# Kernel optimization log

Measured on AMD Instinct MI355X. Metric: run time of the kernel, lower is better.

The kernel has to match this reference:

```python
import jax, jax.numpy as jnp
import numpy as np

NEG_SLOPE = 0.2

def gat_conv(x, src, dst, W, a_src, a_dst, bias, num_nodes, heads, out_ch, concat):
    # x: [N, Fin]; W: [Fin, heads*out_ch]; a_src/a_dst: [heads, out_ch]
    h = (x @ W).reshape(num_nodes, heads, out_ch)            # [N,H,C]
    alpha_s = jnp.einsum('nhc,hc->nh', h, a_src)             # [N,H]
    alpha_d = jnp.einsum('nhc,hc->nh', h, a_dst)             # [N,H]
    e = alpha_s[src] + alpha_d[dst]                          # [E,H]
    e = jnp.where(e > 0, e, NEG_SLOPE * e)                   # LeakyReLU
    # segment softmax over incoming edges per destination node
    m = jax.ops.segment_max(e, dst, num_segments=num_nodes)  # [N,H]
    m = jnp.where(jnp.isfinite(m), m, 0.0)
    ee = jnp.exp(e - m[dst])                                 # [E,H]
    s = jax.ops.segment_sum(ee, dst, num_segments=num_nodes) # [N,H]
    alpha = ee / (s[dst] + 1e-16)                            # [E,H]
    out = jax.ops.segment_sum(h[src] * alpha[:, :, None], dst,
                              num_segments=num_nodes)        # [N,H,C]
    if concat:
        out = out.reshape(num_nodes, heads * out_ch)
    else:
        out = out.mean(axis=1)
    return out + bias


def setup_inputs() -> dict:
    key = jax.random.key(0)
    ks = jax.random.split(key, 10)
    N, E = 50000, 800000
    EMB, HID, HEADS, REPR = 128, 128, 8, 64
    C1 = HID // HEADS  # 16
    x = jax.random.normal(ks[0], (N, EMB), dtype=jnp.float32)
    edge_index = jax.random.randint(ks[1], (2, E), 0, N, dtype=jnp.int32)
    sc = 1.0 / np.sqrt(EMB)
    W1 = jax.random.normal(ks[2], (EMB, HEADS * C1), dtype=jnp.float32) * sc
    a1_src = jax.random.normal(ks[3], (HEADS, C1), dtype=jnp.float32) * 0.1
    a1_dst = jax.random.normal(ks[4], (HEADS, C1), dtype=jnp.float32) * 0.1
    b1 = jnp.zeros((HID,), dtype=jnp.float32)
    sc2 = 1.0 / np.sqrt(HID)
    W2 = jax.random.normal(ks[5], (HID, REPR), dtype=jnp.float32) * sc2
    a2_src = jax.random.normal(ks[6], (1, REPR), dtype=jnp.float32) * 0.1
    a2_dst = jax.random.normal(ks[7], (1, REPR), dtype=jnp.float32) * 0.1
    b2 = jnp.zeros((REPR,), dtype=jnp.float32)
    return {"x": x, "edge_index": edge_index,
            "W1": W1, "a1_src": a1_src, "a1_dst": a1_dst, "b1": b1,
            "W2": W2, "a2_src": a2_src, "a2_dst": a2_dst, "b2": b2}


def reference(x, edge_index, W1, a1_src, a1_dst, b1, W2, a2_src, a2_dst, b2):
    N = x.shape[0]
    # PyG GATConv adds self-loops by default
    loops = jnp.arange(N, dtype=edge_index.dtype)
    src = jnp.concatenate([edge_index[0], loops])
    dst = jnp.concatenate([edge_index[1], loops])
    # eval mode: F.dropout(p=0.6) is identity
    h = gat_conv(x, src, dst, W1, a1_src, a1_dst, b1, N,
                 heads=8, out_ch=16, concat=True)
    h = jax.nn.elu(h)
    out = gat_conv(h, src, dst, W2, a2_src, a2_dst, b2, N,
                   heads=1, out_ch=64, concat=True)
    return out
```

## Files before the change

### kernel.cpp

```cpp
#include <hip/hip_runtime.h>
#include <hip/hip_fp16.h>
#include <math.h>


typedef _Float16 f16x8 __attribute__((ext_vector_type(8)));
typedef float f32x4 __attribute__((ext_vector_type(4)));

#define NCHUNK 32
#define MAXBDIV 8192

__device__ __forceinline__ float leaky_exp(float e) {
    e = (e > 0.f) ? e : 0.2f * e;
    return __expf(e);
}

__device__ __forceinline__ void acc16(float w, float4 hv0, float4 hv1,
                                      float* __restrict__ acc) {
    const __half2* p0 = (const __half2*)&hv0;
    const __half2* p1 = (const __half2*)&hv1;
#pragma unroll
    for (int k = 0; k < 4; k++) {
        float2 f = __half22float2(p0[k]);
        acc[2 * k] += w * f.x;
        acc[2 * k + 1] += w * f.y;
    }
#pragma unroll
    for (int k = 0; k < 4; k++) {
        float2 f = __half22float2(p1[k]);
        acc[8 + 2 * k] += w * f.x;
        acc[8 + 2 * k + 1] += w * f.y;
    }
}

__device__ __forceinline__ void acc8(float w, float4 hv,
                                     float* __restrict__ acc) {
    const __half2* hp = (const __half2*)&hv;
#pragma unroll
    for (int k = 0; k < 4; k++) {
        float2 f = __half22float2(hp[k]);
        acc[2 * k] += w * f.x;
        acc[2 * k + 1] += w * f.y;
    }
}

__global__ __launch_bounds__(256) void augw_kernel(const float* __restrict__ W1,
                                                   const float* __restrict__ a1s,
                                                   const float* __restrict__ a1d,
                                                   const float* __restrict__ W2,
                                                   const float* __restrict__ a2s,
                                                   const float* __restrict__ a2d,
                                                   _Float16* __restrict__ W1t,
                                                   _Float16* __restrict__ W2t,
                                                   int* __restrict__ bucketCnt) {
    int t = threadIdx.x;
    if (blockIdx.x == 0) {
        if (t < 128) bucketCnt[t] = 0;
        for (int i = t; i < 144 * 128; i += 256) {
            int c = i >> 7, k = i & 127;
            float v;
            if (c < 128) {
                v = W1[k * 128 + c];
            } else if (c < 136) {
                int h = c - 128; v = 0.f;
#pragma unroll
                for (int j = 0; j < 16; j++) v += W1[k * 128 + h * 16 + j] * a1s[h * 16 + j];
            } else {
                int h = c - 136; v = 0.f;
#pragma unroll
                for (int j = 0; j < 16; j++) v += W1[k * 128 + h * 16 + j] * a1d[h * 16 + j];
            }
            W1t[c * 128 + k] = (_Float16)v;
        }
    } else {
        for (int i = t; i < 80 * 128; i += 256) {
            int c = i >> 7, k = i & 127;
            float v = 0.f;
            if (c < 64) {
                v = W2[k * 64 + c];
            } else if (c == 64) {
                for (int j = 0; j < 64; j++) v += W2[k * 64 + j] * a2s[j];
            } else if (c == 65) {
                for (int j = 0; j < 64; j++) v += W2[k * 64 + j] * a2d[j];
            }
            W2t[c * 128 + k] = (_Float16)v;
        }
    }
}

__global__ __launch_bounds__(256) void gemm1_bucket_kernel(
        const float* __restrict__ x, const _Float16* __restrict__ W1t,
        __half* __restrict__ h1, float* __restrict__ als,
        float* __restrict__ ald, int N, int gridG1,
        const int* __restrict__ src, const int* __restrict__ dst, int E,
        int* __restrict__ bucketCnt, unsigned* __restrict__ pairs) {
    __shared__ _Float16 Xs[64 * 136];
    int t = threadIdx.x;
    if ((int)blockIdx.x >= gridG1) {
        int* lcnt = (int*)Xs;
        int* lbase = lcnt + 8;
        if (t < 8) lcnt[t] = 0;
        __syncthreads();
        int bid = blockIdx.x - gridG1;
        int bdiv = (N + 7) >> 3;
        int i0 = (bid * 256 + t) * 4;
        int s_[4], d_[4], bk[4], rk[4];
        int nv = 0;
        if (i0 + 3 < E) {
            int4 d4 = *(const int4*)(dst + i0);
            int4 s4 = *(const int4*)(src + i0);
            s_[0] = s4.x; s_[1] = s4.y; s_[2] = s4.z; s_[3] = s4.w;
            d_[0] = d4.x; d_[1] = d4.y; d_[2] = d4.z; d_[3] = d4.w;
            nv = 4;
        } else {
            for (int k = i0; k < E && nv < 4; k++) {
                s_[nv] = src[k]; d_[nv] = dst[k]; nv++;
            }
        }
        int lane = t & 63;
        unsigned long long below = (lane == 0) ? 0ULL : (~0ULL >> (64 - lane));
#pragma unroll
        for (int u = 0; u < 4; u++) {
            bool v = (u < nv);
            int d = v ? d_[u] : 0;
            int b = d / bdiv;
            unsigned long long m0 = __ballot(b & 1);
            unsigned long long m1 = __ballot(b & 2);
            unsigned long long m2 = __ballot(b & 4);
            unsigned long long vm = __ballot(v);
            unsigned long long me = ((b & 1) ? m0 : ~m0) & ((b & 2) ? m1 : ~m1) &
                                    ((b & 4) ? m2 : ~m2) & vm;
            int leader = __ffsll((unsigned long long)me) - 1;
            int ldr = (leader < 0) ? 0 : leader;
            int cnt = __popcll(me);
            int rank = __popcll(me & below);
            int base = 0;
            if (v && lane == leader) base = atomicAdd(&lcnt[b], cnt);
            base = __shfl(base, ldr);
            bk[u] = b;
            rk[u] = base + rank;
        }
        __syncthreads();
        if (t < 8) lbase[t] = atomicAdd(&bucketCnt[t * 16], lcnt[t]);
        __syncthreads();
#pragma unroll 4
        for (int k = 0; k < nv; k++) {
            unsigned dlocal = (unsigned)(d_[k] - bk[k] * ((N + 7) >> 3));
            pairs[(size_t)bk[k] * E + lbase[bk[k]] + rk[k]] =
                (dlocal << 16) | (unsigned)s_[k];
        }
        return;
    }
    int row0 = blockIdx.x * 64;
    for (int i = t; i < 2048; i += 256) {
        int r = i >> 5, c4 = i & 31;
        int gr = row0 + r;
        float4 v = make_float4(0.f, 0.f, 0.f, 0.f);
        if (gr < N) v = *(const float4*)(x + (size_t)gr * 128 + c4 * 4);
        _Float16* dp = Xs + r * 136 + c4 * 4;
        dp[0] = (_Float16)v.x; dp[1] = (_Float16)v.y;
        dp[2] = (_Float16)v.z; dp[3] = (_Float16)v.w;
    }
    __syncthreads();
    int w = t >> 6, L = t & 63, m = L & 15, quad = L >> 4;
    f32x4 acc[9];
#pragma unroll
    for (int f = 0; f < 9; f++) acc[f] = (f32x4){0.f, 0.f, 0.f, 0.f};
    const _Float16* Arow = Xs + (w * 16 + m) * 136 + quad * 8;
    const _Float16* Brow = W1t + m * 128 + quad * 8;
#pragma unroll
    for (int kt = 0; kt < 4; kt++) {
        f16x8 a = *(const f16x8*)(Arow + kt * 32);
#pragma unroll
        for (int f = 0; f < 9; f++) {
            f16x8 b = *(const f16x8*)(Brow + f * 2048 + kt * 32);
            acc[f] = __builtin_amdgcn_mfma_f32_16x16x32_f16(a, b, acc[f], 0, 0, 0);
        }
    }
    int nbase = row0 + w * 16 + quad * 4;
#pragma unroll
    for (int r = 0; r < 4; r++) {
        int n = nbase + r;
        if (n < N) {
            __half* hrow = h1 + (size_t)n * 128 + m;
#pragma unroll
            for (int f = 0; f < 8; f++) hrow[f * 16] = __float2half(acc[f][r]);
            float v = acc[8][r];
            if (m < 8) als[n * 8 + m] = v;
            else ald[n * 8 + (m - 8)] = v;
        }
    }
}

__global__ __launch_bounds__(256) void subhist_kernel(
        const int* __restrict__ bucketCnt, const unsigned* __restrict__ pairs,
        int E, int N, int* __restrict__ subcnt) {
    __shared__ int hist[MAXBDIV];
    int t = threadIdx.x;
    int b = blockIdx.x & 7;
    int j = blockIdx.x >> 3;
    int bdiv = (N + 7) >> 3;
    for (int i = t; i < bdiv; i += 256) hist[i] = 0;
    __syncthreads();
    int cnt = bucketCnt[b * 16];
    int chunk = (cnt + NCHUNK - 1) / NCHUNK;
    int lo = j * chunk;
    int hi = min(lo + chunk, cnt);
    const unsigned* plist = pairs + (size_t)b * E;
    for (int i = lo + t; i < hi; i += 256) {
        atomicAdd(&hist[plist[i] >> 16], 1);
    }
    __syncthreads();
    int* out = subcnt + (size_t)(b * NCHUNK + j) * bdiv;
    for (int i = t; i < bdiv; i += 256) out[i] = hist[i];
}

__global__ __launch_bounds__(256) void scan1_kernel(const int* __restrict__ subcnt,
                                                    int N,
                                                    int* __restrict__ rowstart,
                                                    int* __restrict__ blocksum) {
    __shared__ int tmp[256];
    int t = threadIdx.x;
    int i = blockIdx.x * 256 + t;
    int bdiv = (N + 7) >> 3;
    int v = 0;
    if (i < N) {
        int b = i / bdiv;
        int local = i - b * bdiv;
        const int* sc = subcnt + (size_t)b * NCHUNK * bdiv + local;
#pragma unroll
        for (int j = 0; j < NCHUNK; j++) v += sc[(size_t)j * bdiv];
    }
    tmp[t] = v;
    __syncthreads();
    for (int off = 1; off < 256; off <<= 1) {
        int x = (t >= off) ? tmp[t - off] : 0;
        __syncthreads();
        tmp[t] += x;
        __syncthreads();
    }
    if (i < N) rowstart[i] = tmp[t] - v;
    if (t == 255) blocksum[blockIdx.x] = tmp[t];
}

__global__ __launch_bounds__(256) void scan23_kernel(int* __restrict__ rowstart,
                                                     const int* __restrict__ blocksum,
                                                     int nb,
                                                     int* __restrict__ subcnt,
                                                     int N, int E) {
    __shared__ int sdata[256];
    int t = threadIdx.x;
    int bx = blockIdx.x;
    sdata[t] = (t < nb && t < bx) ? blocksum[t] : 0;
    __syncthreads();
#pragma unroll
    for (int off = 128; off > 0; off >>= 1) {
        if (t < off) sdata[t] += sdata[t + off];
        __syncthreads();
    }
    int offset = sdata[0];
    int i = bx * 256 + t;
    int bdiv = (N + 7) >> 3;
    if (i < N) {
        int v = rowstart[i] + offset;
        rowstart[i] = v;
        int b = i / bdiv;
        int local = i - b * bdiv;
        int* sc = subcnt + (size_t)b * NCHUNK * bdiv + local;
        int c = v;
#pragma unroll
        for (int j = 0; j < NCHUNK; j++) {
            int cj = sc[(size_t)j * bdiv];
            sc[(size_t)j * bdiv] = c;
            c += cj;
        }
    } else if (i == N) {
        rowstart[N] = E;
    }
}

__global__ __launch_bounds__(256) void scatter_kernel(
        const int* __restrict__ bucketCnt, const unsigned* __restrict__ pairs,
        int E, int N, const int* __restrict__ subcnt, int* __restrict__ esrc) {
    __shared__ int lcur[MAXBDIV];
    int t = threadIdx.x;
    int b = blockIdx.x & 7;
    int j = blockIdx.x >> 3;
    int bdiv = (N + 7) >> 3;
    const int* base = subcnt + (size_t)(b * NCHUNK + j) * bdiv;
    for (int i = t; i < bdiv; i += 256) lcur[i] = base[i];
    __syncthreads();
    int cnt = bucketCnt[b * 16];
    int chunk = (cnt + NCHUNK - 1) / NCHUNK;
    int lo = j * chunk;
    int hi = min(lo + chunk, cnt);
    const unsigned* plist = pairs + (size_t)b * E;
    for (int i = lo + t; i < hi; i += 256) {
        unsigned p = plist[i];
        int pos = atomicAdd(&lcur[p >> 16], 1);
        esrc[pos] = (int)(p & 0xFFFFu);
    }
}

__global__ __launch_bounds__(256) void agg1_gemm2_kernel(
        const __half* __restrict__ h1, const float* __restrict__ als,
        const float* __restrict__ ald, const int* __restrict__ rowstart,
        const int* __restrict__ esrc, const float* __restrict__ b1,
        const _Float16* __restrict__ W2t, __half* __restrict__ h2,
        float* __restrict__ al2s, float* __restrict__ al2d, int N) {
    __shared__ _Float16 actS[32 * 136];
    int t = threadIdx.x;
    int lane = t & 63;
    int grp = lane >> 3;
    int q = lane & 7;
    int bdiv = (N + 7) >> 3;
    int lrow = (t >> 6) * 8 + grp;
    int ln = (blockIdx.x >> 3) * 32 + lrow;
    int n = (blockIdx.x & 7) * bdiv + ln;
    bool valid = (ln < bdiv) && (n < N);
    const float4* h1v = (const float4*)h1;
    float acc[16];
#pragma unroll
    for (int k = 0; k < 16; k++) acc[k] = 0.f;
    float wsum = 0.f;
    int beg = 0, end = 0;
    float adv = 0.f;
    if (valid) {
        adv = ald[n * 8 + q];
        float wself = leaky_exp(als[n * 8 + q] + adv);
        wsum = wself;
        acc16(wself, h1v[(size_t)n * 16 + 2 * q], h1v[(size_t)n * 16 + 2 * q + 1], acc);
        beg = rowstart[n];
        end = rowstart[n + 1];
    }
    int j = beg;
    int s0 = 0, s1 = 0, s2 = 0, s3 = 0;
    if (j + 4 <= end) {
        s0 = esrc[j]; s1 = esrc[j + 1]; s2 = esrc[j + 2]; s3 = esrc[j + 3];
    }
    for (; j + 4 <= end; ) {
        float4 a0 = h1v[(size_t)s0 * 16 + 2 * q], b0 = h1v[(size_t)s0 * 16 + 2 * q + 1];
        float4 a1 = h1v[(size_t)s1 * 16 + 2 * q], b1v = h1v[(size_t)s1 * 16 + 2 * q + 1];
        float4 a2 = h1v[(size_t)s2 * 16 + 2 * q], b2 = h1v[(size_t)s2 * 16 + 2 * q + 1];
        float4 a3 = h1v[(size_t)s3 * 16 + 2 * q], b3 = h1v[(size_t)s3 * 16 + 2 * q + 1];
        float e0 = als[s0 * 8 + q], e1 = als[s1 * 8 + q];
        float e2 = als[s2 * 8 + q], e3 = als[s3 * 8 + q];
        int jn = j + 4;
        bool more = (jn + 4 <= end);
        int u0 = more ? esrc[jn]     : 0;
        int u1 = more ? esrc[jn + 1] : 0;
        int u2 = more ? esrc[jn + 2] : 0;
        int u3 = more ? esrc[jn + 3] : 0;
        float w0 = leaky_exp(e0 + adv), w1 = leaky_exp(e1 + adv);
        float w2 = leaky_exp(e2 + adv), w3 = leaky_exp(e3 + adv);
        wsum += (w0 + w1) + (w2 + w3);
        acc16(w0, a0, b0, acc);
        acc16(w1, a1, b1v, acc);
        acc16(w2, a2, b2, acc);
        acc16(w3, a3, b3, acc);
        s0 = u0; s1 = u1; s2 = u2; s3 = u3;
        j = jn;
    }
    for (; j < end; j++) {
        int s = esrc[j];
        float w = leaky_exp(als[s * 8 + q] + adv);
        wsum += w;
        acc16(w, h1v[(size_t)s * 16 + 2 * q], h1v[(size_t)s * 16 + 2 * q + 1], acc);
    }
    __align__(16) __half2 po[8];
    if (valid) {
        float inv = 1.f / (wsum + 1e-16f);
        const float* bf = b1 + q * 16;
#pragma unroll
        for (int k = 0; k < 8; k++) {
            float o0 = acc[2 * k] * inv + bf[2 * k];
            float o1 = acc[2 * k + 1] * inv + bf[2 * k + 1];
            o0 = (o0 > 0.f) ? o0 : (__expf(o0) - 1.f);
            o1 = (o1 > 0.f) ? o1 : (__expf(o1) - 1.f);
            po[k] = __floats2half2_rn(o0, o1);
        }
    } else {
#pragma unroll
        for (int k = 0; k < 8; k++) po[k] = __floats2half2_rn(0.f, 0.f);
    }
    *(float4*)(actS + lrow * 136 + q * 16) = ((float4*)po)[0];
    *(float4*)(actS + lrow * 136 + q * 16 + 8) = ((float4*)po)[1];
    __syncthreads();
    int w4w = t >> 6;
    int m = lane & 15, quad = lane >> 4;
    int rt = w4w & 1;
    int ctbase = (w4w < 2) ? 0 : 1;
    f32x4 acc2[3];
#pragma unroll
    for (int f = 0; f < 3; f++) acc2[f] = (f32x4){0.f, 0.f, 0.f, 0.f};
    const _Float16* Arow2 = actS + (rt * 16 + m) * 136 + quad * 8;
    const _Float16* Brow2 = W2t + m * 128 + quad * 8;
#pragma unroll
    for (int kt = 0; kt < 4; kt++) {
        f16x8 a = *(const f16x8*)(Arow2 + kt * 32);
#pragma unroll
        for (int f = 0; f < 3; f++) {
            int ctf = ctbase + 2 * f;
            if (ctf < 5) {
                f16x8 bb = *(const f16x8*)(Brow2 + ctf * 2048 + kt * 32);
                acc2[f] = __builtin_amdgcn_mfma_f32_16x16x32_f16(a, bb, acc2[f], 0, 0, 0);
            }
        }
    }
    int secbase = (blockIdx.x & 7) * bdiv;
    int lnbase = (blockIdx.x >> 3) * 32 + rt * 16 + quad * 4;
#pragma unroll
    for (int r = 0; r < 4; r++) {
        int ln2 = lnbase + r;
        int n2 = secbase + ln2;
        if (ln2 < bdiv && n2 < N) {
#pragma unroll
            for (int f = 0; f < 3; f++) {
                int ctf = ctbase + 2 * f;
                if (ctf < 4) {
                    h2[(size_t)n2 * 64 + ctf * 16 + m] = __float2half(acc2[f][r]);
                } else if (ctf == 4) {
                    if (m == 0) al2s[n2] = acc2[f][r];
                    else if (m == 1) al2d[n2] = acc2[f][r];
                }
            }
        }
    }
}

__global__ __launch_bounds__(256) void agg2_kernel(const __half* __restrict__ h2,
                                                   const float* __restrict__ al2s,
                                                   const float* __restrict__ al2d,
                                                   const int* __restrict__ rowstart,
                                                   const int* __restrict__ esrc,
                                                   const float* __restrict__ b2,
                                                   float* __restrict__ out, int N) {
    int t = threadIdx.x;
    int lane = t & 63;
    int grp = lane >> 3;
    int q = lane & 7;
    int bdiv = (N + 7) >> 3;
    int ln = (blockIdx.x >> 3) * 32 + (t >> 6) * 8 + grp;
    if (ln >= bdiv) return;
    int n = (blockIdx.x & 7) * bdiv + ln;
    if (n >= N) return;
    const float4* h2v = (const float4*)h2;
    float adv = al2d[n];
    float acc[8];
#pragma unroll
    for (int k = 0; k < 8; k++) acc[k] = 0.f;
    float wsum = 0.f;
    {
        float w = leaky_exp(al2s[n] + adv);
        wsum += w;
        acc8(w, h2v[(size_t)n * 8 + q], acc);
    }
    int beg = rowstart[n], end = rowstart[n + 1];
    int j = beg;
    int s0 = 0, s1 = 0, s2 = 0, s3 = 0;
    if (j + 4 <= end) {
        s0 = esrc[j]; s1 = esrc[j + 1]; s2 = esrc[j + 2]; s3 = esrc[j + 3];
    }
    for (; j + 4 <= end; ) {
        float4 a0 = h2v[(size_t)s0 * 8 + q];
        float4 a1 = h2v[(size_t)s1 * 8 + q];
        float4 a2 = h2v[(size_t)s2 * 8 + q];
        float4 a3 = h2v[(size_t)s3 * 8 + q];
        float e0 = al2s[s0], e1 = al2s[s1], e2 = al2s[s2], e3 = al2s[s3];
        int jn = j + 4;
        bool more = (jn + 4 <= end);
        int u0 = more ? esrc[jn]     : 0;
        int u1 = more ? esrc[jn + 1] : 0;
        int u2 = more ? esrc[jn + 2] : 0;
        int u3 = more ? esrc[jn + 3] : 0;
        float w0 = leaky_exp(e0 + adv), w1 = leaky_exp(e1 + adv);
        float w2 = leaky_exp(e2 + adv), w3 = leaky_exp(e3 + adv);
        wsum += (w0 + w1) + (w2 + w3);
        acc8(w0, a0, acc);
        acc8(w1, a1, acc);
        acc8(w2, a2, acc);
        acc8(w3, a3, acc);
        s0 = u0; s1 = u1; s2 = u2; s3 = u3;
        j = jn;
    }
    for (; j < end; j++) {
        int s = esrc[j];
        float w = leaky_exp(al2s[s] + adv);
        wsum += w;
        acc8(w, h2v[(size_t)s * 8 + q], acc);
    }
    float inv = 1.f / (wsum + 1e-16f);
    const float* bf = b2 + q * 8;
    float4* ov = (float4*)(out + (size_t)n * 64 + q * 8);
    ov[0] = make_float4(acc[0] * inv + bf[0], acc[1] * inv + bf[1],
                        acc[2] * inv + bf[2], acc[3] * inv + bf[3]);
    ov[1] = make_float4(acc[4] * inv + bf[4], acc[5] * inv + bf[5],
                        acc[6] * inv + bf[6], acc[7] * inv + bf[7]);
}

extern "C" void kernel_launch(void* const* d_in, const int* in_sizes, int n_in,
                              void* d_out, int out_size, void* d_ws, size_t ws_size,
                              hipStream_t stream) {
    (void)n_in; (void)out_size; (void)ws_size;
    const float* x   = (const float*)d_in[0];
    const int*   ei  = (const int*)d_in[1];
    const float* W1  = (const float*)d_in[2];
    const float* a1s = (const float*)d_in[3];
    const float* a1d = (const float*)d_in[4];
    const float* b1  = (const float*)d_in[5];
    const float* W2  = (const float*)d_in[6];
    const float* a2s = (const float*)d_in[7];
    const float* a2d = (const float*)d_in[8];
    const float* b2  = (const float*)d_in[9];
    float* out = (float*)d_out;

    const int N = in_sizes[0] / 128;
    const int E = in_sizes[1] / 2;
    const int* src = ei;
    const int* dst = ei + E;
    const int bdiv = (N + 7) / 8;

    char* wp = (char*)d_ws;
    auto alloc = [&](size_t bytes) -> void* {
        void* p = (void*)wp;
        wp += (bytes + 255) & ~(size_t)255;
        return p;
    };
    __half* h1   = (__half*)alloc((size_t)N * 128 * 2);
    __half* h2   = (__half*)alloc((size_t)N * 64 * 2 + 64 * 256);
    float* al1s = (float*)alloc((size_t)N * 8 * 4);
    float* al1d = (float*)alloc((size_t)N * 8 * 4);
    float* al2s = (float*)alloc((size_t)N * 4);
    float* al2d = (float*)alloc((size_t)N * 4);
    int* bucketCnt = (int*)alloc(8 * 16 * 4);
    int* subcnt   = (int*)alloc((size_t)8 * NCHUNK * bdiv * 4);
    int* rowstart = (int*)alloc((size_t)(N + 1) * 4);
    int* esrc     = (int*)alloc((size_t)E * 4);
    unsigned* pairs = (unsigned*)alloc((size_t)8 * E * 4);
    int* blocksum = (int*)alloc(256 * 4);
    _Float16* W1t = (_Float16*)alloc(144 * 128 * 2);
    _Float16* W2t = (_Float16*)alloc(80 * 128 * 2);

    const int nbScan = (N + 255) / 256;
    const int gridH  = (E + 1023) / 1024;
    const int gridG1 = (N + 63) / 64;
    const int gridAggN = 8 * ((bdiv + 31) / 32);
    const int gridSort = 8 * NCHUNK;

    augw_kernel<<<2, 256, 0, stream>>>(W1, a1s, a1d, W2, a2s, a2d, W1t, W2t,
                                       bucketCnt);
    gemm1_bucket_kernel<<<gridG1 + gridH, 256, 0, stream>>>(
        x, W1t, h1, al1s, al1d, N, gridG1, src, dst, E, bucketCnt, pairs);
    subhist_kernel<<<gridSort, 256, 0, stream>>>(bucketCnt, pairs, E, N, subcnt);
    scan1_kernel<<<nbScan, 256, 0, stream>>>(subcnt, N, rowstart, blocksum);
    scan23_kernel<<<(N + 256) / 256, 256, 0, stream>>>(rowstart, blocksum, nbScan,
                                                       subcnt, N, E);
    scatter_kernel<<<gridSort, 256, 0, stream>>>(bucketCnt, pairs, E, N, subcnt, esrc);

    agg1_gemm2_kernel<<<gridAggN, 256, 0, stream>>>(h1, al1s, al1d, rowstart, esrc,
                                                    b1, W2t, h2, al2s, al2d, N);
    agg2_kernel<<<gridAggN, 256, 0, stream>>>(h2, al2s, al2d, rowstart, esrc, b2, out, N);
}
```

Before: 215.9 us.

## Split each node's edge list across two lane groups in both aggregation kernels

```diff
diff --git a/kernel.cpp b/kernel.cpp
--- a/kernel.cpp
+++ b/kernel.cpp
@@ -307,37 +307,45 @@
         const int* __restrict__ esrc, const float* __restrict__ b1,
         const _Float16* __restrict__ W2t, __half* __restrict__ h2,
         float* __restrict__ al2s, float* __restrict__ al2d, int N) {
-    __shared__ _Float16 actS[32 * 136];
+    __shared__ _Float16 actS[16 * 136];
     int t = threadIdx.x;
     int lane = t & 63;
-    int grp = lane >> 3;
-    int q = lane & 7;
+    int w = t >> 6;
+    int k = lane & 15;
+    int q = k & 7;
+    int half = k >> 3;
     int bdiv = (N + 7) >> 3;
-    int lrow = (t >> 6) * 8 + grp;
-    int ln = (blockIdx.x >> 3) * 32 + lrow;
+    int lrow = w * 4 + (lane >> 4);
+    int ln = (blockIdx.x >> 3) * 16 + lrow;
     int n = (blockIdx.x & 7) * bdiv + ln;
     bool valid = (ln < bdiv) && (n < N);
     const float4* h1v = (const float4*)h1;
     float acc[16];
 #pragma unroll
-    for (int k = 0; k < 16; k++) acc[k] = 0.f;
+    for (int kk = 0; kk < 16; kk++) acc[kk] = 0.f;
     float wsum = 0.f;
-    int beg = 0, end = 0;
+    int hbeg = 0, hend = 0;
     float adv = 0.f;
     if (valid) {
         adv = ald[n * 8 + q];
-        float wself = leaky_exp(als[n * 8 + q] + adv);
-        wsum = wself;
-        acc16(wself, h1v[(size_t)n * 16 + 2 * q], h1v[(size_t)n * 16 + 2 * q + 1], acc);
-        beg = rowstart[n];
-        end = rowstart[n + 1];
-    }
-    int j = beg;
+        int beg = rowstart[n], end = rowstart[n + 1];
+        int len = end - beg;
+        int len0 = (len + 1) >> 1;
+        if (half == 0) {
+            hbeg = beg; hend = beg + len0;
+            float wself = leaky_exp(als[n * 8 + q] + adv);
+            wsum = wself;
+            acc16(wself, h1v[(size_t)n * 16 + 2 * q], h1v[(size_t)n * 16 + 2 * q + 1], acc);
+        } else {
+            hbeg = beg + len0; hend = end;
+        }
+    }
+    int j = hbeg;
     int s0 = 0, s1 = 0, s2 = 0, s3 = 0;
-    if (j + 4 <= end) {
+    if (j + 4 <= hend) {
         s0 = esrc[j]; s1 = esrc[j + 1]; s2 = esrc[j + 2]; s3 = esrc[j + 3];
     }
-    for (; j + 4 <= end; ) {
+    for (; j + 4 <= hend; ) {
         float4 a0 = h1v[(size_t)s0 * 16 + 2 * q], b0 = h1v[(size_t)s0 * 16 + 2 * q + 1];
         float4 a1 = h1v[(size_t)s1 * 16 + 2 * q], b1v = h1v[(size_t)s1 * 16 + 2 * q + 1];
         float4 a2 = h1v[(size_t)s2 * 16 + 2 * q], b2 = h1v[(size_t)s2 * 16 + 2 * q + 1];
@@ -345,7 +353,7 @@
         float e0 = als[s0 * 8 + q], e1 = als[s1 * 8 + q];
         float e2 = als[s2 * 8 + q], e3 = als[s3 * 8 + q];
         int jn = j + 4;
-        bool more = (jn + 4 <= end);
+        bool more = (jn + 4 <= hend);
         int u0 = more ? esrc[jn]     : 0;
         int u1 = more ? esrc[jn + 1] : 0;
         int u2 = more ? esrc[jn + 2] : 0;
@@ -360,68 +368,62 @@
         s0 = u0; s1 = u1; s2 = u2; s3 = u3;
         j = jn;
     }
-    for (; j < end; j++) {
+    for (; j < hend; j++) {
         int s = esrc[j];
-        float w = leaky_exp(als[s * 8 + q] + adv);
-        wsum += w;
-        acc16(w, h1v[(size_t)s * 16 + 2 * q], h1v[(size_t)s * 16 + 2 * q + 1], acc);
-    }
+        float ww = leaky_exp(als[s * 8 + q] + adv);
+        wsum += ww;
+        acc16(ww, h1v[(size_t)s * 16 + 2 * q], h1v[(size_t)s * 16 + 2 * q + 1], acc);
+    }
+    wsum += __shfl_xor(wsum, 8);
+#pragma unroll
+    for (int kk = 0; kk < 16; kk++) acc[kk] += __shfl_xor(acc[kk], 8);
     __align__(16) __half2 po[8];
     if (valid) {
         float inv = 1.f / (wsum + 1e-16f);
         const float* bf = b1 + q * 16;
 #pragma unroll
-        for (int k = 0; k < 8; k++) {
-            float o0 = acc[2 * k] * inv + bf[2 * k];
-            float o1 = acc[2 * k + 1] * inv + bf[2 * k + 1];
+        for (int kk = 0; kk < 8; kk++) {
+            float o0 = acc[2 * kk] * inv + bf[2 * kk];
+            float o1 = acc[2 * kk + 1] * inv + bf[2 * kk + 1];
             o0 = (o0 > 0.f) ? o0 : (__expf(o0) - 1.f);
             o1 = (o1 > 0.f) ? o1 : (__expf(o1) - 1.f);
-            po[k] = __floats2half2_rn(o0, o1);
+            po[kk] = __floats2half2_rn(o0, o1);
         }
     } else {
 #pragma unroll
-        for (int k = 0; k < 8; k++) po[k] = __floats2half2_rn(0.f, 0.f);
-    }
-    *(float4*)(actS + lrow * 136 + q * 16) = ((float4*)po)[0];
-    *(float4*)(actS + lrow * 136 + q * 16 + 8) = ((float4*)po)[1];
-    __syncthreads();
-    int w4w = t >> 6;
+        for (int kk = 0; kk < 8; kk++) po[kk] = __floats2half2_rn(0.f, 0.f);
+    }
+    if (half == 0) {
+        *(float4*)(actS + lrow * 136 + q * 16) = ((float4*)po)[0];
+        *(float4*)(actS + lrow * 136 + q * 16 + 8) = ((float4*)po)[1];
+    }
+    __syncthreads();
     int m = lane & 15, quad = lane >> 4;
-    int rt = w4w & 1;
-    int ctbase = (w4w < 2) ? 0 : 1;
-    f32x4 acc2[3];
-#pragma unroll
-    for (int f = 0; f < 3; f++) acc2[f] = (f32x4){0.f, 0.f, 0.f, 0.f};
-    const _Float16* Arow2 = actS + (rt * 16 + m) * 136 + quad * 8;
+    f32x4 acc2a = (f32x4){0.f, 0.f, 0.f, 0.f};
+    f32x4 acc2b = (f32x4){0.f, 0.f, 0.f, 0.f};
+    const _Float16* Arow2 = actS + m * 136 + quad * 8;
     const _Float16* Brow2 = W2t + m * 128 + quad * 8;
 #pragma unroll
     for (int kt = 0; kt < 4; kt++) {
         f16x8 a = *(const f16x8*)(Arow2 + kt * 32);
-#pragma unroll
-        for (int f = 0; f < 3; f++) {
-            int ctf = ctbase + 2 * f;
-            if (ctf < 5) {
-                f16x8 bb = *(const f16x8*)(Brow2 + ctf * 2048 + kt * 32);
-                acc2[f] = __builtin_amdgcn_mfma_f32_16x16x32_f16(a, bb, acc2[f], 0, 0, 0);
-            }
+        f16x8 bb = *(const f16x8*)(Brow2 + w * 2048 + kt * 32);
+        acc2a = __builtin_amdgcn_mfma_f32_16x16x32_f16(a, bb, acc2a, 0, 0, 0);
+        if (w == 0) {
+            f16x8 bc = *(const f16x8*)(Brow2 + 4 * 2048 + kt * 32);
+            acc2b = __builtin_amdgcn_mfma_f32_16x16x32_f16(a, bc, acc2b, 0, 0, 0);
         }
     }
     int secbase = (blockIdx.x & 7) * bdiv;
-    int lnbase = (blockIdx.x >> 3) * 32 + rt * 16 + quad * 4;
+    int lnbase = (blockIdx.x >> 3) * 16 + quad * 4;
 #pragma unroll
     for (int r = 0; r < 4; r++) {
         int ln2 = lnbase + r;
         int n2 = secbase + ln2;
         if (ln2 < bdiv && n2 < N) {
-#pragma unroll
-            for (int f = 0; f < 3; f++) {
-                int ctf = ctbase + 2 * f;
-                if (ctf < 4) {
-                    h2[(size_t)n2 * 64 + ctf * 16 + m] = __float2half(acc2[f][r]);
-                } else if (ctf == 4) {
-                    if (m == 0) al2s[n2] = acc2[f][r];
-                    else if (m == 1) al2d[n2] = acc2[f][r];
-                }
+            h2[(size_t)n2 * 64 + w * 16 + m] = __float2half(acc2a[r]);
+            if (w == 0) {
+                if (m == 0) al2s[n2] = acc2b[r];
+                else if (m == 1) al2d[n2] = acc2b[r];
             }
         }
     }
@@ -436,38 +438,49 @@
                                                    float* __restrict__ out, int N) {
     int t = threadIdx.x;
     int lane = t & 63;
-    int grp = lane >> 3;
-    int q = lane & 7;
+    int w = t >> 6;
+    int k = lane & 15;
+    int q = k & 7;
+    int half = k >> 3;
     int bdiv = (N + 7) >> 3;
-    int ln = (blockIdx.x >> 3) * 32 + (t >> 6) * 8 + grp;
-    if (ln >= bdiv) return;
+    int lrow = w * 4 + (lane >> 4);
+    int ln = (blockIdx.x >> 3) * 16 + lrow;
     int n = (blockIdx.x & 7) * bdiv + ln;
-    if (n >= N) return;
+    bool valid = (ln < bdiv) && (n < N);
     const float4* h2v = (const float4*)h2;
-    float adv = al2d[n];
     float acc[8];
 #pragma unroll
-    for (int k = 0; k < 8; k++) acc[k] = 0.f;
+    for (int kk = 0; kk < 8; kk++) acc[kk] = 0.f;
     float wsum = 0.f;
-    {
-        float w = leaky_exp(al2s[n] + adv);
-        wsum += w;
-        acc8(w, h2v[(size_t)n * 8 + q], acc);
-    }
-    int beg = rowstart[n], end = rowstart[n + 1];
-    int j = beg;
+    int hbeg = 0, hend = 0;
+    float adv = 0.f;
+    if (valid) {
+        adv = al2d[n];
+        int beg = rowstart[n], end = rowstart[n + 1];
+        int len = end - beg;
+        int len0 = (len + 1) >> 1;
+        if (half == 0) {
+            hbeg = beg; hend = beg + len0;
+            float wself = leaky_exp(al2s[n] + adv);
+            wsum = wself;
+            acc8(wself, h2v[(size_t)n * 8 + q], acc);
+        } else {
+            hbeg = beg + len0; hend = end;
+        }
+    }
+    int j = hbeg;
     int s0 = 0, s1 = 0, s2 = 0, s3 = 0;
-    if (j + 4 <= end) {
+    if (j + 4 <= hend) {
         s0 = esrc[j]; s1 = esrc[j + 1]; s2 = esrc[j + 2]; s3 = esrc[j + 3];
     }
-    for (; j + 4 <= end; ) {
+    for (; j + 4 <= hend; ) {
         float4 a0 = h2v[(size_t)s0 * 8 + q];
         float4 a1 = h2v[(size_t)s1 * 8 + q];
         float4 a2 = h2v[(size_t)s2 * 8 + q];
         float4 a3 = h2v[(size_t)s3 * 8 + q];
         float e0 = al2s[s0], e1 = al2s[s1], e2 = al2s[s2], e3 = al2s[s3];
         int jn = j + 4;
-        bool more = (jn + 4 <= end);
+        bool more = (jn + 4 <= hend);
         int u0 = more ? esrc[jn]     : 0;
         int u1 = more ? esrc[jn + 1] : 0;
         int u2 = more ? esrc[jn + 2] : 0;
@@ -482,19 +495,24 @@
         s0 = u0; s1 = u1; s2 = u2; s3 = u3;
         j = jn;
     }
-    for (; j < end; j++) {
+    for (; j < hend; j++) {
         int s = esrc[j];
-        float w = leaky_exp(al2s[s] + adv);
-        wsum += w;
-        acc8(w, h2v[(size_t)s * 8 + q], acc);
-    }
-    float inv = 1.f / (wsum + 1e-16f);
-    const float* bf = b2 + q * 8;
-    float4* ov = (float4*)(out + (size_t)n * 64 + q * 8);
-    ov[0] = make_float4(acc[0] * inv + bf[0], acc[1] * inv + bf[1],
-                        acc[2] * inv + bf[2], acc[3] * inv + bf[3]);
-    ov[1] = make_float4(acc[4] * inv + bf[4], acc[5] * inv + bf[5],
-                        acc[6] * inv + bf[6], acc[7] * inv + bf[7]);
+        float ww = leaky_exp(al2s[s] + adv);
+        wsum += ww;
+        acc8(ww, h2v[(size_t)s * 8 + q], acc);
+    }
+    wsum += __shfl_xor(wsum, 8);
+#pragma unroll
+    for (int kk = 0; kk < 8; kk++) acc[kk] += __shfl_xor(acc[kk], 8);
+    if (valid && half == 0) {
+        float inv = 1.f / (wsum + 1e-16f);
+        const float* bf = b2 + q * 8;
+        float4* ov = (float4*)(out + (size_t)n * 64 + q * 8);
+        ov[0] = make_float4(acc[0] * inv + bf[0], acc[1] * inv + bf[1],
+                            acc[2] * inv + bf[2], acc[3] * inv + bf[3]);
+        ov[1] = make_float4(acc[4] * inv + bf[4], acc[5] * inv + bf[5],
+                            acc[6] * inv + bf[6], acc[7] * inv + bf[7]);
+    }
 }
 
 extern "C" void kernel_launch(void* const* d_in, const int* in_sizes, int n_in,
@@ -543,7 +561,7 @@
     const int nbScan = (N + 255) / 256;
     const int gridH  = (E + 1023) / 1024;
     const int gridG1 = (N + 63) / 64;
-    const int gridAggN = 8 * ((bdiv + 31) / 32);
+    const int gridAggN = 8 * ((bdiv + 15) / 16);
     const int gridSort = 8 * NCHUNK;
 
     augw_kernel<<<2, 256, 0, stream>>>(W1, a1s, a1d, W2, a2s, a2d, W1t, W2t,
```

New measurement: 219.0 us. No clear change (+1.5%).
